# Optimization experiments

Hardware: AMD Instinct MI355X
Metric: run time of the kernel (lower is better)

## Reference

```python
import jax, jax.numpy as jnp
import numpy as np
import math

VOCAB = 128000
D_MODEL = 1024
CUTOFFS = [20000, 60000, VOCAB]  # cluster boundaries (last = vocab_size)
B, S = 8, 4096


def setup_inputs() -> dict:
    key = jax.random.key(0)
    ks = jax.random.split(key, 6)
    input_ids = jax.random.randint(ks[0], (B, S), 0, VOCAB)
    # cluster 0: ids [0, 20000), dim 1024, padding_idx=0 -> zero row
    emb0 = jax.random.normal(ks[1], (20000, 1024), jnp.float32)
    emb0 = emb0.at[0].set(0.0)
    # cluster 1: ids [20000, 60000), dim 256 (= 1024 // 4**1)
    emb1 = jax.random.normal(ks[2], (40000, 256), jnp.float32)
    # cluster 2: ids [60000, 128000), dim 64 (= 1024 // 4**2)
    emb2 = jax.random.normal(ks[3], (68000, 64), jnp.float32)
    # nn.Linear(emb_dim, d_model, bias=False): weight shape [d_model, emb_dim]
    proj1 = jax.random.normal(ks[4], (1024, 256), jnp.float32) * 0.02
    proj2 = jax.random.normal(ks[5], (1024, 64), jnp.float32) * 0.02
    return {"input_ids": input_ids, "emb0": emb0, "emb1": emb1, "emb2": emb2,
            "proj1": proj1, "proj2": proj2}


def reference(input_ids, emb0, emb1, emb2, proj1, proj2):
    d_model = emb0.shape[1]
    starts = [0, CUTOFFS[0], CUTOFFS[1]]
    ends = CUTOFFS
    tables = [emb0, emb1, emb2]
    projs = [None, proj1, proj2]
    out = jnp.zeros(input_ids.shape + (d_model,), jnp.float32)
    for start, end, tab, proj in zip(starts, ends, tables, projs):
        mask = (input_ids >= start) & (input_ids < end)          # [B,S]
        local = jnp.clip(input_ids - start, 0, tab.shape[0] - 1)  # in-range gather ids
        e = tab[local]                                            # [B,S,emb_dim]
        if proj is not None:
            e = jnp.einsum('bse,de->bsd', e, proj)                # project to d_model
        else:
            # padding_idx=0: row is zero; mask keeps grad out of row 0 too
            e = e * (input_ids != 0)[..., None].astype(e.dtype)
        out = out + jnp.where(mask[..., None], e, 0.0)            # masked scatter
    return out * math.sqrt(d_model)
```

## Files before the change

### kernel.cpp

```cpp
#include <hip/hip_runtime.h>
#include <hip/hip_bf16.h>


typedef __attribute__((ext_vector_type(4))) float        float4v;
typedef __attribute__((ext_vector_type(8))) short        short8;
typedef __attribute__((ext_vector_type(2))) unsigned int uint2v;
typedef __attribute__((ext_vector_type(2))) int          int2v;

#define D_MODEL 1024

__device__ __forceinline__ short f2bf(float x) {
    unsigned u = __builtin_bit_cast(unsigned, x);
    unsigned r = u + 0x7fffu + ((u >> 16) & 1u);
    return (short)(r >> 16);
}

__device__ __forceinline__ short8 cvt8(float4v a, float4v b) {
    short8 r;
    r[0] = f2bf(a[0]); r[1] = f2bf(a[1]); r[2] = f2bf(a[2]); r[3] = f2bf(a[3]);
    r[4] = f2bf(b[0]); r[5] = f2bf(b[1]); r[6] = f2bf(b[2]); r[7] = f2bf(b[3]);
    return r;
}

__device__ __forceinline__ uint2v pack4(float4v v) {
    uint2v r;
    r[0] = (unsigned)(unsigned short)f2bf(v[0]) | ((unsigned)(unsigned short)f2bf(v[1]) << 16);
    r[1] = (unsigned)(unsigned short)f2bf(v[2]) | ((unsigned)(unsigned short)f2bf(v[3]) << 16);
    return r;
}

__global__ __launch_bounds__(1024)
void prep_k(const int* __restrict__ ids, int n, int pb,
            int* __restrict__ cnt,
            int2v* __restrict__ l0, int2v* __restrict__ l1, int2v* __restrict__ l2,
            const float* __restrict__ proj1, const float* __restrict__ proj2,
            short8* __restrict__ p1bf, short8* __restrict__ p2bf)
{
    const int b = blockIdx.x;
    if (b >= pb) {
        int bb = b - pb;
        if (bb < 32) {
            int t    = bb * 1024 + threadIdx.x;
            int lane = t & 63;
            int ks32 = (t >> 6) & 7;
            int nt   = t >> 9;
            int nrow = nt * 16 + (lane & 15);
            int k0   = ks32 * 32 + (lane >> 4) * 8;
            const float* s = proj1 + nrow * 256 + k0;
            p1bf[t] = cvt8(*(const float4v*)s, *(const float4v*)(s + 4));
        } else {
            int t    = (bb - 32) * 1024 + threadIdx.x;
            int lane = t & 63;
            int ks32 = (t >> 6) & 1;
            int nt   = t >> 7;
            int nrow = nt * 16 + (lane & 15);
            int k0   = ks32 * 32 + (lane >> 4) * 8;
            const float* s = proj2 + nrow * 64 + k0;
            p2bf[t] = cvt8(*(const float4v*)s, *(const float4v*)(s + 4));
        }
        return;
    }

    __shared__ int s_wcnt[16][3];
    __shared__ int s_wbase[16][3];
    __shared__ int s_base[3];

    const int tid  = threadIdx.x;
    const int wave = tid >> 6;
    const int lane = tid & 63;
    const int i    = b * 1024 + tid;

    int id = (i < n) ? ids[i] : -1;
    bool is0 = (i < n) && (id < 20000);
    bool is1 = (i < n) && (id >= 20000) && (id < 60000);
    bool is2 = (i < n) && (id >= 60000);
    unsigned long long ltmask = (lane == 0) ? 0ull : (~0ull >> (64 - lane));

    unsigned long long m0 = __ballot(is0);
    unsigned long long m1 = __ballot(is1);
    unsigned long long m2 = __ballot(is2);
    if (lane == 0) {
        s_wcnt[wave][0] = __popcll(m0);
        s_wcnt[wave][1] = __popcll(m1);
        s_wcnt[wave][2] = __popcll(m2);
    }
    __syncthreads();

    if (tid < 3) {
        const int c = tid;
        int run = 0;
#pragma unroll
        for (int w = 0; w < 16; w++) { s_wbase[w][c] = run; run += s_wcnt[w][c]; }
        const int gidx = (c == 0) ? 2 : (c - 1);
        s_base[c] = atomicAdd(&cnt[gidx], run);
    }
    __syncthreads();

    if (is0) l0[s_base[0] + s_wbase[wave][0] + __popcll(m0 & ltmask)] = (int2v){i, id};
    if (is1) l1[s_base[1] + s_wbase[wave][1] + __popcll(m1 & ltmask)] = (int2v){i, id - 20000};
    if (is2) l2[s_base[2] + s_wbase[wave][2] + __popcll(m2 & ltmask)] = (int2v){i, id - 60000};
}

template<int K>
__device__ __forceinline__
void gemm_tile(int tile,
               const float* __restrict__ table,
               const short8* __restrict__ pbf,
               const int2v* __restrict__ list,
               int count,
               float* __restrict__ out,
               int2v* s_tl, short* s_a, float* s_t)
{
    constexpr int PK = K + 8;
    constexpr int KS = K / 32;
    const int m_base = tile * 32;
    const int tid = threadIdx.x;
    if (tid < 32) {
        int m = m_base + tid;
        s_tl[tid] = (m < count) ? list[m] : (int2v){-1, 0};
    }
    __syncthreads();

    {
        const int row = tid >> 4;
        const int c   = tid & 15;
        const float* src = table + (size_t)s_tl[row][1] * K + c * (K / 16);
        short*       dst = s_a + row * PK + c * (K / 16);
        if constexpr (K == 256) {
            const float4v* s4 = (const float4v*)src;
            float4v f0 = s4[0], f1 = s4[1], f2 = s4[2], f3 = s4[3];
            uint2v* d2 = (uint2v*)dst;
            d2[0] = pack4(f0); d2[1] = pack4(f1);
            d2[2] = pack4(f2); d2[3] = pack4(f3);
        } else {
            float4v f0 = *(const float4v*)src;
            *(uint2v*)dst = pack4(f0);
        }
    }
    __syncthreads();

    const int lane = tid & 63;
    const int wave = tid >> 6;
    const int col  = lane & 15;
    const int quad = lane >> 4;

    const short* arow0 = s_a + col * PK        + quad * 8;
    const short* arow1 = s_a + (col + 16) * PK + quad * 8;

    float4v acc0[8], acc1[8];
#pragma unroll
    for (int i = 0; i < 8; i++) {
        acc0[i] = (float4v){0.f, 0.f, 0.f, 0.f};
        acc1[i] = (float4v){0.f, 0.f, 0.f, 0.f};
    }

#pragma unroll
    for (int ks32 = 0; ks32 < KS; ks32++) {
        short8 a0 = *(const short8*)(arow0 + ks32 * 32);
        short8 a1 = *(const short8*)(arow1 + ks32 * 32);
        const short8* bp = pbf + ((size_t)(wave * 8) * KS + ks32) * 64 + lane;
#pragma unroll
        for (int nt = 0; nt < 8; nt++) {
            short8 b = bp[(size_t)nt * KS * 64];
            acc0[nt] = __builtin_amdgcn_mfma_f32_16x16x32_bf16(a0, b, acc0[nt], 0, 0, 0);
            acc1[nt] = __builtin_amdgcn_mfma_f32_16x16x32_bf16(a1, b, acc1[nt], 0, 0, 0);
        }
    }

    __syncthreads();
    float* tsc = s_t + wave * (8 * 132);
    const int c4   = (lane & 31) * 4;
    const int half = lane >> 5;
    const int qh   = quad >> 1;
    const int lr0  = (quad & 1) * 4;

#pragma unroll
    for (int g = 0; g < 4; g++) {
        if (qh == (g & 1)) {
#pragma unroll
            for (int nt = 0; nt < 8; nt++)
#pragma unroll
                for (int r = 0; r < 4; r++) {
                    float v = (g < 2) ? acc0[nt][r] : acc1[nt][r];
                    tsc[(lr0 + r) * 132 + nt * 16 + col] = v * 32.0f;
                }
        }
        __syncthreads();
#pragma unroll
        for (int s = 0; s < 4; s++) {
            int lr = s * 2 + half;
            int R  = g * 8 + lr;
            float4v v = *(const float4v*)&tsc[lr * 132 + c4];
            if (m_base + R < count) {
                int tok = s_tl[R][0];
                *(float4v*)(out + (size_t)tok * D_MODEL + wave * 128 + c4) = v;
            }
        }
        __syncthreads();
    }
}

__device__ __forceinline__
void copy_item(int item, const int2v* __restrict__ l0, int count0,
               const float* __restrict__ emb0, float* __restrict__ out)
{
    int r = item * 8 + (threadIdx.x >> 6);
    if (r < count0) {
        int2v tl = l0[r];
        const float4v* src = (const float4v*)(emb0 + (size_t)tl[1] * D_MODEL);
        float4v*       dst = (float4v*)(out + (size_t)tl[0] * D_MODEL);
        int c = threadIdx.x & 63;
        float4v v0 = src[c], v1 = src[c + 64], v2 = src[c + 128], v3 = src[c + 192];
        dst[c]       = v0 * 32.0f;
        dst[c + 64]  = v1 * 32.0f;
        dst[c + 128] = v2 * 32.0f;
        dst[c + 192] = v3 * 32.0f;
    }
}

__global__ __launch_bounds__(512)
void fused_main(const float* __restrict__ emb0,
                const float* __restrict__ emb1,
                const float* __restrict__ emb2,
                const short8* __restrict__ p1bf,
                const short8* __restrict__ p2bf,
                const int2v* __restrict__ l0,
                const int2v* __restrict__ l1,
                const int2v* __restrict__ l2,
                const int* __restrict__ cnt,
                float* __restrict__ out)
{
    __shared__ int2v s_tl[32];
    __shared__ __align__(16) char s_buf[8 * 8 * 132 * 4];
    short* s_a = (short*)s_buf;
    float* s_t = (float*)s_buf;

    const int c1 = cnt[0];
    const int c2 = cnt[1];
    const int c0 = cnt[2];
    const int t1 = (c1 + 31) >> 5;
    const int t2 = (c2 + 31) >> 5;
    const int tc = (c0 + 7) >> 3;
    const int total = t1 + t2 + tc;

    for (int w = blockIdx.x; w < total; w += gridDim.x) {
        if (w < t1) {
            gemm_tile<256>(w, emb1, p1bf, l1, c1, out, s_tl, s_a, s_t);
        } else if (w < t1 + t2) {
            gemm_tile<64>(w - t1, emb2, p2bf, l2, c2, out, s_tl, s_a, s_t);
        } else {
            copy_item(w - t1 - t2, l0, c0, emb0, out);
        }
    }
}

extern "C" void kernel_launch(void* const* d_in, const int* in_sizes, int n_in,
                              void* d_out, int out_size, void* d_ws, size_t ws_size,
                              hipStream_t stream)
{
    const int*   ids   = (const int*)  d_in[0];
    const float* emb0  = (const float*)d_in[1];
    const float* emb1  = (const float*)d_in[2];
    const float* emb2  = (const float*)d_in[3];
    const float* proj1 = (const float*)d_in[4];
    const float* proj2 = (const float*)d_in[5];
    float*       out   = (float*)d_out;
    const int n = in_sizes[0];

    int*   cnt  = (int*)d_ws;
    int2v* l0   = (int2v*)((char*)d_ws + 256);
    int2v* l1   = l0 + n;
    int2v* l2   = l1 + n;
    size_t poff = (256 + (size_t)3 * n * 8 + 255) & ~(size_t)255;
    short8* p1bf = (short8*)((char*)d_ws + poff);
    short8* p2bf = p1bf + 32768;

    const int pb = (n + 1023) / 1024;

    hipMemsetAsync(cnt, 0, 4 * sizeof(int), stream);
    prep_k<<<pb + 32 + 8, 1024, 0, stream>>>(ids, n, pb, cnt, l0, l1, l2,
                                             proj1, proj2, p1bf, p2bf);
    fused_main<<<1024, 512, 0, stream>>>(emb0, emb1, emb2,
                                         p1bf, p2bf, l0, l1, l2, cnt, out);
}
```

Before: 266.2 us.

## Split GEMM tiles across two half-width blocks of 256 threads

Each 32-token GEMM tile is now split into two work items that each compute half of the 1024 output columns, with blocks shrunk from 512 to 256 threads (4 waves). Copy items also shrink to 4 rows per item. Staging the A tile into shared memory is redone with 8 threads per row, and shared memory is resized for the smaller block. This gives finer-grained work and more resident blocks. The cost is that each 32-row A tile is gathered and bf16-converted twice, once per half.

New measurement: 273.3 us. +2.7%, slower.

```diff
diff --git a/kernel.cpp b/kernel.cpp
--- a/kernel.cpp
+++ b/kernel.cpp
@@ -103,7 +103,7 @@
 
 template<int K>
 __device__ __forceinline__
-void gemm_tile(int tile,
+void gemm_item(int tile, int dimh,
                const float* __restrict__ table,
                const short8* __restrict__ pbf,
                const int2v* __restrict__ list,
@@ -122,19 +122,20 @@
     __syncthreads();
 
     {
-        const int row = tid >> 4;
-        const int c   = tid & 15;
-        const float* src = table + (size_t)s_tl[row][1] * K + c * (K / 16);
-        short*       dst = s_a + row * PK + c * (K / 16);
+        const int row = tid >> 3;
+        const int c   = tid & 7;
+        const float* src = table + (size_t)s_tl[row][1] * K + c * (K / 8);
+        short*       dst = s_a + row * PK + c * (K / 8);
         if constexpr (K == 256) {
             const float4v* s4 = (const float4v*)src;
-            float4v f0 = s4[0], f1 = s4[1], f2 = s4[2], f3 = s4[3];
             uint2v* d2 = (uint2v*)dst;
-            d2[0] = pack4(f0); d2[1] = pack4(f1);
-            d2[2] = pack4(f2); d2[3] = pack4(f3);
+#pragma unroll
+            for (int j = 0; j < 8; j++) d2[j] = pack4(s4[j]);
         } else {
-            float4v f0 = *(const float4v*)src;
-            *(uint2v*)dst = pack4(f0);
+            const float4v* s4 = (const float4v*)src;
+            uint2v* d2 = (uint2v*)dst;
+            d2[0] = pack4(s4[0]);
+            d2[1] = pack4(s4[1]);
         }
     }
     __syncthreads();
@@ -146,6 +147,7 @@
 
     const short* arow0 = s_a + col * PK        + quad * 8;
     const short* arow1 = s_a + (col + 16) * PK + quad * 8;
+    const int ntile0 = dimh * 32 + wave * 8;
 
     float4v acc0[8], acc1[8];
 #pragma unroll
@@ -158,7 +160,7 @@
     for (int ks32 = 0; ks32 < KS; ks32++) {
         short8 a0 = *(const short8*)(arow0 + ks32 * 32);
         short8 a1 = *(const short8*)(arow1 + ks32 * 32);
-        const short8* bp = pbf + ((size_t)(wave * 8) * KS + ks32) * 64 + lane;
+        const short8* bp = pbf + ((size_t)ntile0 * KS + ks32) * 64 + lane;
 #pragma unroll
         for (int nt = 0; nt < 8; nt++) {
             short8 b = bp[(size_t)nt * KS * 64];
@@ -173,6 +175,7 @@
     const int half = lane >> 5;
     const int qh   = quad >> 1;
     const int lr0  = (quad & 1) * 4;
+    const int obase = dimh * 512 + wave * 128;
 
 #pragma unroll
     for (int g = 0; g < 4; g++) {
@@ -193,7 +196,7 @@
             float4v v = *(const float4v*)&tsc[lr * 132 + c4];
             if (m_base + R < count) {
                 int tok = s_tl[R][0];
-                *(float4v*)(out + (size_t)tok * D_MODEL + wave * 128 + c4) = v;
+                *(float4v*)(out + (size_t)tok * D_MODEL + obase + c4) = v;
             }
         }
         __syncthreads();
@@ -204,7 +207,7 @@
 void copy_item(int item, const int2v* __restrict__ l0, int count0,
                const float* __restrict__ emb0, float* __restrict__ out)
 {
-    int r = item * 8 + (threadIdx.x >> 6);
+    int r = item * 4 + (threadIdx.x >> 6);
     if (r < count0) {
         int2v tl = l0[r];
         const float4v* src = (const float4v*)(emb0 + (size_t)tl[1] * D_MODEL);
@@ -218,7 +221,7 @@
     }
 }
 
-__global__ __launch_bounds__(512)
+__global__ __launch_bounds__(256)
 void fused_main(const float* __restrict__ emb0,
                 const float* __restrict__ emb1,
                 const float* __restrict__ emb2,
@@ -231,25 +234,26 @@
                 float* __restrict__ out)
 {
     __shared__ int2v s_tl[32];
-    __shared__ __align__(16) char s_buf[8 * 8 * 132 * 4];
+    __shared__ __align__(16) char s_buf[32 * 264 * 2];
     short* s_a = (short*)s_buf;
     float* s_t = (float*)s_buf;
 
     const int c1 = cnt[0];
     const int c2 = cnt[1];
     const int c0 = cnt[2];
-    const int t1 = (c1 + 31) >> 5;
-    const int t2 = (c2 + 31) >> 5;
-    const int tc = (c0 + 7) >> 3;
-    const int total = t1 + t2 + tc;
+    const int g1 = ((c1 + 31) >> 5) * 2;
+    const int g2 = ((c2 + 31) >> 5) * 2;
+    const int tc = (c0 + 3) >> 2;
+    const int total = g1 + g2 + tc;
 
     for (int w = blockIdx.x; w < total; w += gridDim.x) {
-        if (w < t1) {
-            gemm_tile<256>(w, emb1, p1bf, l1, c1, out, s_tl, s_a, s_t);
-        } else if (w < t1 + t2) {
-            gemm_tile<64>(w - t1, emb2, p2bf, l2, c2, out, s_tl, s_a, s_t);
+        if (w < g1) {
+            gemm_item<256>(w >> 1, w & 1, emb1, p1bf, l1, c1, out, s_tl, s_a, s_t);
+        } else if (w < g1 + g2) {
+            int u = w - g1;
+            gemm_item<64>(u >> 1, u & 1, emb2, p2bf, l2, c2, out, s_tl, s_a, s_t);
         } else {
-            copy_item(w - t1 - t2, l0, c0, emb0, out);
+            copy_item(w - g1 - g2, l0, c0, emb0, out);
         }
     }
 }
@@ -280,6 +284,6 @@
     hipMemsetAsync(cnt, 0, 4 * sizeof(int), stream);
     prep_k<<<pb + 32 + 8, 1024, 0, stream>>>(ids, n, pb, cnt, l0, l1, l2,
                                              proj1, proj2, p1bf, p2bf);
-    fused_main<<<1024, 512, 0, stream>>>(emb0, emb1, emb2,
+    fused_main<<<1024, 256, 0, stream>>>(emb0, emb1, emb2,
                                          p1bf, p2bf, l0, l1, l2, cnt, out);
 }
```
